# Performance work log

Hardware: AMD Instinct MI355X
Metric: run time of the kernel (lower is better)

Reference implementation:

```python
import jax, jax.numpy as jnp
import numpy as np
from jax.scipy.linalg import expm

ETA = 0.1
B, N = 8192, 64


def setup_inputs() -> dict:
    key = jax.random.key(0)
    k_r, k_g = jax.random.split(key)
    # R must be strictly positive: torch.log is ELEMENTWISE log in the original.
    # Shift uniform away from 0 so log(R) stays well-conditioned.
    R = jax.random.uniform(k_r, (B, N, N), dtype=jnp.float32, minval=0.1, maxval=1.0)
    grad = jax.random.normal(k_g, (B, N, N), dtype=jnp.float32)
    return {"R": R, "grad": grad}


def reference(R, grad):
    # skew-symmetric part of the gradient: G - G^T
    skew_grad = grad - jnp.swapaxes(grad, -1, -2)          # [B, N, N]
    # elementwise log (matches torch.log, NOT a matrix logarithm)
    update = jnp.log(R) - ETA * skew_grad                  # [B, N, N]
    # batched matrix exponential (scaling-and-squaring + Pade)
    new_R = jax.vmap(expm)(update)                         # [B, N, N]
    return new_R
```

## Files before the change

kernel.cpp:

```cpp
#include <hip/hip_runtime.h>
#include <math.h>

#define ETA 0.1f

#define C0 1.0f
#define C1 1.0f
#define C2 0.5f
#define C3 (1.0f/6.0f)
#define C4 (1.0f/24.0f)
#define C5 (1.0f/120.0f)
#define C6 (1.0f/720.0f)
#define C7 (1.0f/5040.0f)
#define C8 (1.0f/40320.0f)
#define C9 (1.0f/362880.0f)

typedef __attribute__((ext_vector_type(8))) short short8;
typedef __attribute__((ext_vector_type(4))) float f32x4;

__device__ __forceinline__ int swzF(int r, int cc) { return r * 64 + 4 * (cc ^ (r & 15)); }

__device__ __forceinline__ int rmI(int r, int c) {
    return r * 64 + 8 * ((c >> 3) ^ (r & 7)) + (c & 7);
}
__device__ __forceinline__ int cmI(int r, int c) {
    return c * 64 + 8 * ((r >> 3) ^ (c & 7)) + (r & 7);
}

__device__ __forceinline__ void splitbf(float x, unsigned short& h, unsigned short& l) {
    unsigned u = __float_as_uint(x);
    unsigned r = u + 0x7FFFu + ((u >> 16) & 1u);
    h = (unsigned short)(r >> 16);
    float d = x - __uint_as_float(r & 0xFFFF0000u);
    l = (unsigned short)(__float_as_uint(d) >> 16);
}
__device__ __forceinline__ float bf2f(unsigned short h) {
    return __uint_as_float(((unsigned)h) << 16);
}

__device__ __forceinline__ void mmstage(
    const unsigned short* Ah, const unsigned short* Al,
    const unsigned short* Bh, const unsigned short* Bl,
    unsigned short* Oh, unsigned short* Ol,
    unsigned short* ORh, unsigned short* ORl,
    const float* bmf, float cI, float cB, bool cmIsT0,
    int wv, int lane)
{
    const int n16 = lane & 15;
    const int q = lane >> 4;
    const int mrow = 16 * wv + n16;

    short8 ah[2], al[2], bh[4][2], bl[4][2];
#pragma unroll
    for (int ks = 0; ks < 2; ++ks) {
        int k0 = 32 * ks + 8 * q;
        int ia = rmI(mrow, k0);
        ah[ks] = *(const short8*)(Ah + ia);
        al[ks] = *(const short8*)(Al + ia);
#pragma unroll
        for (int t4 = 0; t4 < 4; ++t4) {
            int ib = cmI(k0, 16 * t4 + n16);
            bh[t4][ks] = *(const short8*)(Bh + ib);
            bl[t4][ks] = *(const short8*)(Bl + ib);
        }
    }

    f32x4 acc[4] = {{0.f,0.f,0.f,0.f},{0.f,0.f,0.f,0.f},{0.f,0.f,0.f,0.f},{0.f,0.f,0.f,0.f}};
#pragma unroll
    for (int ks = 0; ks < 2; ++ks) {
#pragma unroll
        for (int t4 = 0; t4 < 4; ++t4)
            acc[t4] = __builtin_amdgcn_mfma_f32_16x16x32_bf16(ah[ks], bh[t4][ks], acc[t4], 0, 0, 0);
#pragma unroll
        for (int t4 = 0; t4 < 4; ++t4)
            acc[t4] = __builtin_amdgcn_mfma_f32_16x16x32_bf16(al[ks], bl[t4][ks], acc[t4], 0, 0, 0);
#pragma unroll
        for (int t4 = 0; t4 < 4; ++t4)
            acc[t4] = __builtin_amdgcn_mfma_f32_16x16x32_bf16(ah[ks], bl[t4][ks], acc[t4], 0, 0, 0);
#pragma unroll
        for (int t4 = 0; t4 < 4; ++t4)
            acc[t4] = __builtin_amdgcn_mfma_f32_16x16x32_bf16(al[ks], bh[t4][ks], acc[t4], 0, 0, 0);
    }

    const int rbase = 16 * wv + 4 * q;
    float cmv[4][4];
#pragma unroll
    for (int t4 = 0; t4 < 4; ++t4) {
        int c = 16 * t4 + n16;
#pragma unroll
        for (int rg = 0; rg < 4; ++rg) {
            float a = acc[t4][rg];
            if (bmf) {
                float add = cB * bmf[4 * t4 + rg] + ((rbase + rg) == c ? cI : 0.f);
                if (cmIsT0) { cmv[t4][rg] = add; }
                else        { a += add; cmv[t4][rg] = a; acc[t4][rg] = a; }
            } else {
                cmv[t4][rg] = a;
            }
        }
    }

    __syncthreads();

#pragma unroll
    for (int t4 = 0; t4 < 4; ++t4) {
        int c = 16 * t4 + n16;
        {
            unsigned short h[4], l[4];
#pragma unroll
            for (int rg = 0; rg < 4; ++rg) splitbf(cmv[t4][rg], h[rg], l[rg]);
            int io = cmI(rbase, c);
            *(ushort4*)(Oh + io) = make_ushort4(h[0], h[1], h[2], h[3]);
            *(ushort4*)(Ol + io) = make_ushort4(l[0], l[1], l[2], l[3]);
        }
        if (ORh) {
            unsigned short h[4], l[4];
#pragma unroll
            for (int rg = 0; rg < 4; ++rg) splitbf(acc[t4][rg], h[rg], l[rg]);
#pragma unroll
            for (int rg = 0; rg < 4; ++rg) {
                int io = rmI(rbase + rg, c);
                ORh[io] = h[rg];
                ORl[io] = l[rg];
            }
        }
    }
    __syncthreads();
}

__global__ __launch_bounds__(256, 4) void meg_expm_kernel(
    const float* __restrict__ Rg, const float* __restrict__ Gg,
    float* __restrict__ out)
{
    __shared__ __align__(16) unsigned short sm[16384];
    unsigned short* rmh = sm;
    unsigned short* rml = sm + 4096;
    unsigned short* cmh = sm + 8192;
    unsigned short* cml = sm + 12288;
    float* FBG = (float*)sm;
    float* FBA = (float*)(sm + 8192);
    float* wmax = (float*)sm;

    const int t = threadIdx.x;
    const int wv = t >> 6, lane = t & 63;
    const int tx = t & 15, ty = t >> 4;
    const long long base = (long long)blockIdx.x * 4096;

#pragma unroll
    for (int i = 0; i < 4; ++i) {
        int idx = t + i * 256;
        int r = idx >> 4, cc = idx & 15;
        *(float4*)&FBG[swzF(r, cc)] = ((const float4*)(Gg + base))[idx];
    }
    __syncthreads();

#pragma unroll
    for (int i = 0; i < 4; ++i) {
        int r = 4 * ty + i;
        float4 rv = *(const float4*)&Rg[base + r * 64 + 4 * tx];
        float4 gv = *(const float4*)&FBG[swzF(r, tx)];
        float gt[4];
#pragma unroll
        for (int j = 0; j < 4; ++j)
            gt[j] = FBG[swzF(4 * tx + j, r >> 2) + (r & 3)];
        float4 o;
        o.x = logf(rv.x) - ETA * (gv.x - gt[0]);
        o.y = logf(rv.y) - ETA * (gv.y - gt[1]);
        o.z = logf(rv.z) - ETA * (gv.z - gt[2]);
        o.w = logf(rv.w) - ETA * (gv.w - gt[3]);
        *(float4*)&FBA[swzF(r, tx)] = o;
    }
    __syncthreads();

    {
        int c = 16 * wv + (lane & 15);
        int rq = lane >> 4;
        float cs = 0.f;
#pragma unroll
        for (int rr = 0; rr < 16; ++rr) {
            int r = 16 * rq + rr;
            cs += fabsf(FBA[swzF(r, c >> 2) + (c & 3)]);
        }
        cs += __shfl_xor(cs, 16);
        cs += __shfl_xor(cs, 32);
        cs = fmaxf(cs, __shfl_xor(cs, 8));
        cs = fmaxf(cs, __shfl_xor(cs, 4));
        cs = fmaxf(cs, __shfl_xor(cs, 2));
        cs = fmaxf(cs, __shfl_xor(cs, 1));
        if (lane == 0) wmax[wv] = cs;
    }
    __syncthreads();

    const float nrm = fmaxf(fmaxf(wmax[0], wmax[1]), fmaxf(wmax[2], wmax[3]));
    int s = 0;
    if (nrm > 1.0f) {
        s = (int)ceilf(log2f(nrm));
        if (s > 30) s = 30;
        if (s < 0) s = 0;
    }
    const float scale = exp2f(-(float)s);

    unsigned short abmh[4][4], abml[4][4];
#pragma unroll
    for (int i = 0; i < 4; ++i) {
        int r = 4 * ty + i;
        float4 a = *(const float4*)&FBA[swzF(r, tx)];
        float av[4] = { a.x, a.y, a.z, a.w };
#pragma unroll
        for (int j = 0; j < 4; ++j)
            splitbf(av[j] * scale, abmh[i][j], abml[i][j]);
    }
    __syncthreads();

#pragma unroll
    for (int i = 0; i < 4; ++i) {
        int r = 4 * ty + i;
        *(ushort4*)(rmh + rmI(r, 4 * tx)) = make_ushort4(abmh[i][0], abmh[i][1], abmh[i][2], abmh[i][3]);
        *(ushort4*)(rml + rmI(r, 4 * tx)) = make_ushort4(abml[i][0], abml[i][1], abml[i][2], abml[i][3]);
#pragma unroll
        for (int j = 0; j < 4; ++j) {
            int ic = cmI(r, 4 * tx + j);
            cmh[ic] = abmh[i][j];
            cml[ic] = abml[i][j];
        }
    }
    __syncthreads();

    const int n16 = lane & 15, q = lane >> 4;
    const int rbase = 16 * wv + 4 * q;
    float bmf[16];
#pragma unroll
    for (int t4 = 0; t4 < 4; ++t4) {
        int ib = cmI(rbase, 16 * t4 + n16);
        ushort4 hh = *(const ushort4*)(cmh + ib);
        ushort4 ll = *(const ushort4*)(cml + ib);
        bmf[4 * t4 + 0] = bf2f(hh.x) + bf2f(ll.x);
        bmf[4 * t4 + 1] = bf2f(hh.y) + bf2f(ll.y);
        bmf[4 * t4 + 2] = bf2f(hh.z) + bf2f(ll.z);
        bmf[4 * t4 + 3] = bf2f(hh.w) + bf2f(ll.w);
    }

    mmstage(rmh, rml, cmh, cml, cmh, cml, rmh, rml, bmf, C8, C9, true,  wv, lane);

    mmstage(rmh, rml, cmh, cml, cmh, cml, nullptr, nullptr, bmf, C6, C7, false, wv, lane);
    mmstage(rmh, rml, cmh, cml, cmh, cml, nullptr, nullptr, bmf, C4, C5, false, wv, lane);
    mmstage(rmh, rml, cmh, cml, cmh, cml, nullptr, nullptr, bmf, C2, C3, false, wv, lane);
    mmstage(rmh, rml, cmh, cml, cmh, cml, rmh, rml, bmf, C0, C1, false, wv, lane);

    for (int it = 0; it < s; ++it) {
        bool lastp = (it == s - 1);
        mmstage(rmh, rml, cmh, cml, cmh, cml,
                lastp ? nullptr : rmh, lastp ? nullptr : rml,
                nullptr, 0.f, 0.f, false, wv, lane);
    }

#pragma unroll
    for (int i = 0; i < 4; ++i) {
        int g = i * 256 + t;
        int r = g >> 4, cg = g & 15;
        float ov[4];
#pragma unroll
        for (int j = 0; j < 4; ++j) {
            int c = 4 * cg + j;
            int ic = cmI(r, c);
            ov[j] = bf2f(cmh[ic]) + bf2f(cml[ic]);
        }
        float4 o;
        o.x = ov[0]; o.y = ov[1]; o.z = ov[2]; o.w = ov[3];
        ((float4*)(out + base))[g] = o;
    }
}

extern "C" void kernel_launch(void* const* d_in, const int* in_sizes, int n_in,
                              void* d_out, int out_size, void* d_ws, size_t ws_size,
                              hipStream_t stream) {
    const float* R = (const float*)d_in[0];
    const float* G = (const float*)d_in[1];
    float* o = (float*)d_out;
    const int B = in_sizes[0] / (64 * 64);
    meg_expm_kernel<<<dim3(B), dim3(256), 0, stream>>>(R, G, o);
}
```

Measured before the change: 466.6 us.

## Drop lo*lo MFMA term, vectorize LDS stores, write final stage directly to global

Removes the low-times-low bf16 MFMA product in the split-precision matmul, cutting MFMA work per stage by a quarter. Adds a 4x4 lane transpose via xor shuffles so row-major LDS writes become vectorized ushort4 stores instead of scalar ones, and vectorizes the initial column-major store. The last matmul stage now writes fp32 results straight to global memory, skipping the final LDS round trip and its extra barrier. Dropping lo*lo lowers accuracy slightly, and the direct global stores are uncoalesced scalar writes.

```diff
diff --git a/kernel.cpp b/kernel.cpp
--- a/kernel.cpp
+++ b/kernel.cpp
@@ -37,12 +37,25 @@
     return __uint_as_float(((unsigned)h) << 16);
 }
 
+__device__ __forceinline__ void xpose4(float v[4], int lane) {
+    float s, g;
+    s = (lane & 1) ? v[0] : v[1];  g = __shfl_xor(s, 1);
+    if (lane & 1) v[0] = g; else v[1] = g;
+    s = (lane & 1) ? v[2] : v[3];  g = __shfl_xor(s, 1);
+    if (lane & 1) v[2] = g; else v[3] = g;
+    s = (lane & 2) ? v[0] : v[2];  g = __shfl_xor(s, 2);
+    if (lane & 2) v[0] = g; else v[2] = g;
+    s = (lane & 2) ? v[1] : v[3];  g = __shfl_xor(s, 2);
+    if (lane & 2) v[1] = g; else v[3] = g;
+}
+
 __device__ __forceinline__ void mmstage(
     const unsigned short* Ah, const unsigned short* Al,
     const unsigned short* Bh, const unsigned short* Bl,
     unsigned short* Oh, unsigned short* Ol,
     unsigned short* ORh, unsigned short* ORl,
-    const float* bmf, float cI, float cB, bool cmIsT0,
+    float* gout, long long gbase,
+    const float* bmf, float cI, float cB, bool t0mode,
     int wv, int lane)
 {
     const int n16 = lane & 15;
@@ -72,9 +85,6 @@
             acc[t4] = __builtin_amdgcn_mfma_f32_16x16x32_bf16(ah[ks], bh[t4][ks], acc[t4], 0, 0, 0);
 #pragma unroll
         for (int t4 = 0; t4 < 4; ++t4)
-            acc[t4] = __builtin_amdgcn_mfma_f32_16x16x32_bf16(al[ks], bl[t4][ks], acc[t4], 0, 0, 0);
-#pragma unroll
-        for (int t4 = 0; t4 < 4; ++t4)
             acc[t4] = __builtin_amdgcn_mfma_f32_16x16x32_bf16(ah[ks], bl[t4][ks], acc[t4], 0, 0, 0);
 #pragma unroll
         for (int t4 = 0; t4 < 4; ++t4)
@@ -85,43 +95,72 @@
     float cmv[4][4];
 #pragma unroll
     for (int t4 = 0; t4 < 4; ++t4) {
-        int c = 16 * t4 + n16;
+        const int c = 16 * t4 + n16;
 #pragma unroll
         for (int rg = 0; rg < 4; ++rg) {
             float a = acc[t4][rg];
-            if (bmf) {
-                float add = cB * bmf[4 * t4 + rg] + ((rbase + rg) == c ? cI : 0.f);
-                if (cmIsT0) { cmv[t4][rg] = add; }
-                else        { a += add; cmv[t4][rg] = a; acc[t4][rg] = a; }
+            if (bmf && !t0mode) {
+                a += cB * bmf[4 * t4 + rg] + (((rbase + rg) == c) ? cI : 0.f);
+                acc[t4][rg] = a;
+                cmv[t4][rg] = a;
+            } else if (t0mode) {
+                cmv[t4][rg] = cB * bmf[4 * t4 + rg] + (((rbase + rg) == c) ? cI : 0.f);
             } else {
                 cmv[t4][rg] = a;
             }
         }
     }
 
-    __syncthreads();
-
+    if (gout) {
+        float* gp = gout + gbase;
+#pragma unroll
+        for (int t4 = 0; t4 < 4; ++t4) {
+            const int c = 16 * t4 + n16;
+#pragma unroll
+            for (int rg = 0; rg < 4; ++rg)
+                gp[(rbase + rg) * 64 + c] = cmv[t4][rg];
+        }
+        return;
+    }
+
+    ushort4 cmH[4], cmL[4], rmH[4], rmL[4];
 #pragma unroll
     for (int t4 = 0; t4 < 4; ++t4) {
-        int c = 16 * t4 + n16;
-        {
+        unsigned short h[4], l[4];
+#pragma unroll
+        for (int rg = 0; rg < 4; ++rg) splitbf(cmv[t4][rg], h[rg], l[rg]);
+        cmH[t4] = make_ushort4(h[0], h[1], h[2], h[3]);
+        cmL[t4] = make_ushort4(l[0], l[1], l[2], l[3]);
+    }
+    if (ORh) {
+#pragma unroll
+        for (int t4 = 0; t4 < 4; ++t4) {
+            float v[4] = { acc[t4][0], acc[t4][1], acc[t4][2], acc[t4][3] };
+            xpose4(v, lane);
             unsigned short h[4], l[4];
 #pragma unroll
-            for (int rg = 0; rg < 4; ++rg) splitbf(cmv[t4][rg], h[rg], l[rg]);
-            int io = cmI(rbase, c);
-            *(ushort4*)(Oh + io) = make_ushort4(h[0], h[1], h[2], h[3]);
-            *(ushort4*)(Ol + io) = make_ushort4(l[0], l[1], l[2], l[3]);
-        }
-        if (ORh) {
-            unsigned short h[4], l[4];
-#pragma unroll
-            for (int rg = 0; rg < 4; ++rg) splitbf(acc[t4][rg], h[rg], l[rg]);
-#pragma unroll
-            for (int rg = 0; rg < 4; ++rg) {
-                int io = rmI(rbase + rg, c);
-                ORh[io] = h[rg];
-                ORl[io] = l[rg];
-            }
+            for (int rg = 0; rg < 4; ++rg) splitbf(v[rg], h[rg], l[rg]);
+            rmH[t4] = make_ushort4(h[0], h[1], h[2], h[3]);
+            rmL[t4] = make_ushort4(l[0], l[1], l[2], l[3]);
+        }
+    }
+
+    __syncthreads();
+
+#pragma unroll
+    for (int t4 = 0; t4 < 4; ++t4) {
+        const int io = cmI(rbase, 16 * t4 + n16);
+        *(ushort4*)(Oh + io) = cmH[t4];
+        *(ushort4*)(Ol + io) = cmL[t4];
+    }
+    if (ORh) {
+        const int rowp = rbase + (lane & 3);
+        const int c4b  = 4 * ((lane >> 2) & 3);
+#pragma unroll
+        for (int t4 = 0; t4 < 4; ++t4) {
+            const int io = rmI(rowp, 16 * t4 + c4b);
+            *(ushort4*)(ORh + io) = rmH[t4];
+            *(ushort4*)(ORl + io) = rmL[t4];
         }
     }
     __syncthreads();
@@ -216,12 +255,12 @@
         int r = 4 * ty + i;
         *(ushort4*)(rmh + rmI(r, 4 * tx)) = make_ushort4(abmh[i][0], abmh[i][1], abmh[i][2], abmh[i][3]);
         *(ushort4*)(rml + rmI(r, 4 * tx)) = make_ushort4(abml[i][0], abml[i][1], abml[i][2], abml[i][3]);
-#pragma unroll
-        for (int j = 0; j < 4; ++j) {
-            int ic = cmI(r, 4 * tx + j);
-            cmh[ic] = abmh[i][j];
-            cml[ic] = abml[i][j];
-        }
+    }
+#pragma unroll
+    for (int j = 0; j < 4; ++j) {
+        const int ic = cmI(4 * ty, 4 * tx + j);
+        *(ushort4*)(cmh + ic) = make_ushort4(abmh[0][j], abmh[1][j], abmh[2][j], abmh[3][j]);
+        *(ushort4*)(cml + ic) = make_ushort4(abml[0][j], abml[1][j], abml[2][j], abml[3][j]);
     }
     __syncthreads();
 
@@ -230,43 +269,39 @@
     float bmf[16];
 #pragma unroll
     for (int t4 = 0; t4 < 4; ++t4) {
-        int ib = cmI(rbase, 16 * t4 + n16);
-        ushort4 hh = *(const ushort4*)(cmh + ib);
-        ushort4 ll = *(const ushort4*)(cml + ib);
+        const int ib = cmI(rbase, 16 * t4 + n16);
+        const ushort4 hh = *(const ushort4*)(cmh + ib);
+        const ushort4 ll = *(const ushort4*)(cml + ib);
         bmf[4 * t4 + 0] = bf2f(hh.x) + bf2f(ll.x);
         bmf[4 * t4 + 1] = bf2f(hh.y) + bf2f(ll.y);
         bmf[4 * t4 + 2] = bf2f(hh.z) + bf2f(ll.z);
         bmf[4 * t4 + 3] = bf2f(hh.w) + bf2f(ll.w);
     }
 
-    mmstage(rmh, rml, cmh, cml, cmh, cml, rmh, rml, bmf, C8, C9, true,  wv, lane);
-
-    mmstage(rmh, rml, cmh, cml, cmh, cml, nullptr, nullptr, bmf, C6, C7, false, wv, lane);
-    mmstage(rmh, rml, cmh, cml, cmh, cml, nullptr, nullptr, bmf, C4, C5, false, wv, lane);
-    mmstage(rmh, rml, cmh, cml, cmh, cml, nullptr, nullptr, bmf, C2, C3, false, wv, lane);
-    mmstage(rmh, rml, cmh, cml, cmh, cml, rmh, rml, bmf, C0, C1, false, wv, lane);
+    mmstage(rmh, rml, cmh, cml, cmh, cml, rmh, rml, nullptr, 0,
+            bmf, C8, C9, true, wv, lane);
+
+    mmstage(rmh, rml, cmh, cml, cmh, cml, nullptr, nullptr, nullptr, 0,
+            bmf, C6, C7, false, wv, lane);
+    mmstage(rmh, rml, cmh, cml, cmh, cml, nullptr, nullptr, nullptr, 0,
+            bmf, C4, C5, false, wv, lane);
+    mmstage(rmh, rml, cmh, cml, cmh, cml, nullptr, nullptr, nullptr, 0,
+            bmf, C2, C3, false, wv, lane);
+
+    if (s == 0) {
+        mmstage(rmh, rml, cmh, cml, nullptr, nullptr, nullptr, nullptr, out, base,
+                bmf, C0, C1, false, wv, lane);
+        return;
+    }
+    mmstage(rmh, rml, cmh, cml, cmh, cml, rmh, rml, nullptr, 0,
+            bmf, C0, C1, false, wv, lane);
 
     for (int it = 0; it < s; ++it) {
-        bool lastp = (it == s - 1);
+        const bool last = (it == s - 1);
         mmstage(rmh, rml, cmh, cml, cmh, cml,
-                lastp ? nullptr : rmh, lastp ? nullptr : rml,
+                last ? nullptr : rmh, last ? nullptr : rml,
+                last ? out : nullptr, base,
                 nullptr, 0.f, 0.f, false, wv, lane);
-    }
-
-#pragma unroll
-    for (int i = 0; i < 4; ++i) {
-        int g = i * 256 + t;
-        int r = g >> 4, cg = g & 15;
-        float ov[4];
-#pragma unroll
-        for (int j = 0; j < 4; ++j) {
-            int c = 4 * cg + j;
-            int ic = cmI(r, c);
-            ov[j] = bf2f(cmh[ic]) + bf2f(cml[ic]);
-        }
-        float4 o;
-        o.x = ov[0]; o.y = ov[1]; o.z = ov[2]; o.w = ov[3];
-        ((float4*)(out + base))[g] = o;
     }
 }
 
```

Measured after the change: 474.9 us. About the same (+1.8%).
